# Performance work log

Hardware: AMD Instinct MI355X
Metric: run time of the kernel (lower is better)

The kernel has to match this reference:

```python
import jax, jax.numpy as jnp
import numpy as np

N_HEAD = 16

def setup_inputs() -> dict:
    key = jax.random.key(0)
    kx, kq, kk, kv, kp = jax.random.split(key, 5)
    B, T, C = 4, 2048, 1024
    scale = 1.0 / np.sqrt(C)
    x = jax.random.normal(kx, (B, T, C), dtype=jnp.float32)
    Wq = jax.random.normal(kq, (C, C), dtype=jnp.float32) * scale
    Wk = jax.random.normal(kk, (C, C), dtype=jnp.float32) * scale
    Wv = jax.random.normal(kv, (C, C), dtype=jnp.float32) * scale
    Wp = jax.random.normal(kp, (C, C), dtype=jnp.float32) * scale
    return {"x": x, "Wq": Wq, "Wk": Wk, "Wv": Wv, "Wp": Wp}

def reference(x, Wq, Wk, Wv, Wp):
    B, T, C = x.shape
    H = N_HEAD
    D = C // H
    # projections (nn.Linear, no bias): x @ W^T
    q = (x @ Wq.T).reshape(B, T, H, D).transpose(0, 2, 1, 3)  # [B,H,T,D]
    k = (x @ Wk.T).reshape(B, T, H, D).transpose(0, 2, 1, 3)
    v = (x @ Wv.T).reshape(B, T, H, D).transpose(0, 2, 1, 3)
    att = jnp.einsum('bhqd,bhkd->bhqk', q, k) / jnp.sqrt(jnp.float32(D))
    causal = jnp.tril(jnp.ones((T, T), dtype=bool))
    att = jnp.where(causal, att, -jnp.inf)
    att = jax.nn.softmax(att, axis=-1)
    # dropout p=0.0 -> identity
    y = jnp.einsum('bhqk,bhkd->bhqd', att, v)  # [B,H,T,D]
    y = y.transpose(0, 2, 1, 3).reshape(B, T, C)
    return y @ Wp.T
```

## Files before the change

kernel.cpp:

```cpp
#include <hip/hip_runtime.h>

typedef __bf16 bfrag __attribute__((ext_vector_type(8)));
typedef __bf16 bh4 __attribute__((ext_vector_type(4)));
typedef float f4 __attribute__((ext_vector_type(4)));

#define AS1C(p) (const __attribute__((address_space(1))) void*)(p)
#define AS3(p)  (__attribute__((address_space(3))) void*)(p)

#define QSCALE 0.18033688011112042f

__device__ __forceinline__ void g2l16(const __bf16* g, __bf16* l) {
  __builtin_amdgcn_global_load_lds(AS1C(g), AS3(l), 16, 0, 0);
}

__global__ __launch_bounds__(256) void cvt5(
    const float* __restrict__ s0, const float* __restrict__ s1,
    const float* __restrict__ s2, const float* __restrict__ s3,
    const float* __restrict__ s4,
    __bf16* __restrict__ d0, __bf16* __restrict__ d1, __bf16* __restrict__ d2,
    __bf16* __restrict__ d3, __bf16* __restrict__ d4, long n0, long n1) {
  const float* s; __bf16* d; long n;
  switch (blockIdx.y) {
    case 0: s = s0; d = d0; n = n0; break;
    case 1: s = s1; d = d1; n = n1; break;
    case 2: s = s2; d = d2; n = n1; break;
    case 3: s = s3; d = d3; n = n1; break;
    default: s = s4; d = d4; n = n1; break;
  }
  long i = ((long)blockIdx.x * 256 + threadIdx.x) * 8;
  if (i >= n) return;
  float4 a = *(const float4*)(s + i);
  float4 b = *(const float4*)(s + i + 4);
  bfrag o;
  o[0] = (__bf16)a.x; o[1] = (__bf16)a.y; o[2] = (__bf16)a.z; o[3] = (__bf16)a.w;
  o[4] = (__bf16)b.x; o[5] = (__bf16)b.y; o[6] = (__bf16)b.z; o[7] = (__bf16)b.w;
  *(bfrag*)(d + i) = o;
}

#define BARR __builtin_amdgcn_s_barrier()
#define WAIT_LGKM { asm volatile("s_waitcnt lgkmcnt(0)" ::: "memory"); \
                    __builtin_amdgcn_sched_barrier(0); }
#define WAIT_VM(N) asm volatile("s_waitcnt vmcnt(" #N ")" ::: "memory")

template <int MODE>
__global__ __launch_bounds__(512, 2) void gemm_dp(
    const __bf16* __restrict__ A, const __bf16* __restrict__ Bw,
    __bf16* __restrict__ qb, __bf16* __restrict__ kb,
    __bf16* __restrict__ vt, float* __restrict__ Cf, int K) {
  __shared__ __bf16 lds[73728];
  __bf16* ldsA = lds;
  __bf16* ldsB = lds + 24576;
  const int tid = threadIdx.x;
  const int wave = tid >> 6, lane = tid & 63;
  const int lm = lane & 15, quad = lane >> 4;
  const int wm = wave >> 2, wn = wave & 3;
  const int bm = blockIdx.x * 128, bn = blockIdx.y * 256;
  const int srow = lane >> 3;
  const int scol = ((lane & 7) ^ srow) * 8;
  const int rsw = lm & 7;

#define STG_A9(sl, kt) { \
    const __bf16* gp_ = A + (long)(bm + wave * 16 + srow) * K + (kt) * 64 + scol; \
    __bf16* lp_ = ldsA + (sl) * 8192 + wave * 1024 + lane * 8; \
    g2l16(gp_, lp_); g2l16(gp_ + 8 * K, lp_ + 512); }
#define STG_B9(sl, kt, h) { \
    const __bf16* gp_ = Bw + (long)(bn + (h) * 128 + wave * 16 + srow) * K + (kt) * 64 + scol; \
    __bf16* lp_ = ldsB + (sl) * 16384 + (h) * 8192 + wave * 1024 + lane * 8; \
    g2l16(gp_, lp_); g2l16(gp_ + 8 * K, lp_ + 512); }
#define STG_TILE(sl, kt) { STG_A9(sl, kt); STG_B9(sl, kt, 0); STG_B9(sl, kt, 1); }

#define COMPUTE_HALF(sl) { \
    const __bf16* Ab_ = ldsA + (sl) * 8192 + (wm * 64 + lm) * 64; \
    const __bf16* Bb_ = ldsB + (sl) * 16384 + (wn * 64 + lm) * 64; \
    bfrag af_[4][2], bg_[2][2]; \
    _Pragma("unroll") for (int j_ = 0; j_ < 4; ++j_) \
      _Pragma("unroll") for (int kk_ = 0; kk_ < 2; ++kk_) \
        af_[j_][kk_] = *(const bfrag*)(Ab_ + j_ * 1024 + ((kk_ * 4 + quad) ^ rsw) * 8); \
    _Pragma("unroll") for (int n_ = 0; n_ < 2; ++n_) \
      _Pragma("unroll") for (int kk_ = 0; kk_ < 2; ++kk_) \
        bg_[n_][kk_] = *(const bfrag*)(Bb_ + n_ * 1024 + ((kk_ * 4 + quad) ^ rsw) * 8); \
    WAIT_LGKM; \
    __builtin_amdgcn_s_setprio(1); \
    _Pragma("unroll") for (int j_ = 0; j_ < 4; ++j_) \
      _Pragma("unroll") for (int n_ = 0; n_ < 2; ++n_) \
        _Pragma("unroll") for (int kk_ = 0; kk_ < 2; ++kk_) \
          acc[j_][n_] = __builtin_amdgcn_mfma_f32_16x16x32_bf16( \
              af_[j_][kk_], bg_[n_][kk_], acc[j_][n_], 0, 0, 0); \
    __builtin_amdgcn_s_setprio(0); \
    _Pragma("unroll") for (int n_ = 0; n_ < 2; ++n_) \
      _Pragma("unroll") for (int kk_ = 0; kk_ < 2; ++kk_) \
        bg_[n_][kk_] = *(const bfrag*)(Bb_ + (2 + n_) * 1024 + ((kk_ * 4 + quad) ^ rsw) * 8); \
    WAIT_LGKM; \
    __builtin_amdgcn_s_setprio(1); \
    _Pragma("unroll") for (int j_ = 0; j_ < 4; ++j_) \
      _Pragma("unroll") for (int n_ = 0; n_ < 2; ++n_) \
        _Pragma("unroll") for (int kk_ = 0; kk_ < 2; ++kk_) \
          acc[j_][2 + n_] = __builtin_amdgcn_mfma_f32_16x16x32_bf16( \
              af_[j_][kk_], bg_[n_][kk_], acc[j_][2 + n_], 0, 0, 0); \
    __builtin_amdgcn_s_setprio(0); }

  f4 acc[4][4] = {};
  const int ntiles = K >> 6;
  STG_TILE(0, 0);
  STG_TILE(1, 1);
  WAIT_VM(6);
  BARR;
#pragma unroll 1
  for (int i = 0; i < (ntiles >> 1); ++i) {
    const int e = 2 * i, o = 2 * i + 1;
    const int se = e % 3, so = o % 3;
    if (e + 2 < ntiles) { const int s2 = (e + 2) % 3; STG_TILE(s2, e + 2); }
    COMPUTE_HALF(se);
    if (e + 2 < ntiles) { WAIT_VM(6); } else { WAIT_VM(0); }
    BARR;
    if (o + 2 < ntiles) { const int s2 = (o + 2) % 3; STG_TILE(s2, o + 2); }
    COMPUTE_HALF(so);
    if (o + 2 < ntiles) WAIT_VM(6);
    BARR;
  }

  if (MODE == 1) {
#pragma unroll
    for (int mi = 0; mi < 4; ++mi)
#pragma unroll
      for (int ni = 0; ni < 4; ++ni)
#pragma unroll
        for (int r = 0; r < 4; ++r) {
          long row = bm + wm * 64 + mi * 16 + quad * 4 + r;
          long col = bn + wn * 64 + ni * 16 + lm;
          Cf[row * 1024 + col] = acc[mi][ni][r];
        }
  } else if (bn < 2048) {
    __bf16* dst = (bn < 1024) ? qb : kb;
    const float scl = (bn < 1024) ? QSCALE : 1.0f;
    const int nb = bn & 1023;
#pragma unroll
    for (int mi = 0; mi < 4; ++mi)
#pragma unroll
      for (int ni = 0; ni < 4; ++ni)
#pragma unroll
        for (int r = 0; r < 4; ++r) {
          long row = bm + wm * 64 + mi * 16 + quad * 4 + r;
          long col = nb + wn * 64 + ni * 16 + lm;
          dst[row * 1024 + col] = (__bf16)(acc[mi][ni][r] * scl);
        }
  } else {
#pragma unroll
    for (int mi = 0; mi < 4; ++mi)
#pragma unroll
      for (int ni = 0; ni < 4; ++ni)
#pragma unroll
        for (int r = 0; r < 4; ++r) {
          int d = wn * 64 + ni * 16 + lm;
          int tp = wm * 64 + (quad * 4 + r) * 4 + mi;
          lds[d * 130 + tp] = (__bf16)acc[mi][ni][r];
        }
    __syncthreads();
    const int bloc = bm >> 11;
    const int tloc = bm & 2047;
#pragma unroll
    for (int p = 0; p < 8; ++p) {
      int d = (tid >> 4) + p * 32;
      int c = (tid & 15) * 8;
      long dglob = (bn - 2048) + d;
      *(bfrag*)(vt + ((long)bloc * 1024 + dglob) * 2048 + tloc + c) =
          *(const bfrag*)(lds + d * 130 + c);
    }
  }
}

template <bool A_F32, bool OUT_F32>
__global__ __launch_bounds__(256) void gemm_bt_cv(
    const void* __restrict__ Ap, const float* __restrict__ Bp,
    void* __restrict__ Cp, int M, int N, int K, float scl) {
  __shared__ __bf16 As[128 * 32];
  __shared__ __bf16 Bs[128 * 32];
  const int tid = threadIdx.x;
  const int lane = tid & 63, wave = tid >> 6;
  const int lm = lane & 15, quad = lane >> 4;
  const int bm = blockIdx.x * 128, bn = blockIdx.y * 128;
  const int wr = (wave >> 1) * 64, wc = (wave & 1) * 64;
  const int e0 = tid * 16, sr = e0 >> 5, sc = e0 & 31;
  f4 acc[4][4] = {};
  for (int k0 = 0; k0 < K; k0 += 32) {
    if (A_F32) {
      const float4* ga = (const float4*)((const float*)Ap + (long)(bm + sr) * K + k0 + sc);
#pragma unroll
      for (int j = 0; j < 4; ++j) {
        float4 v = ga[j];
        As[sr * 32 + sc + j * 4 + 0] = (__bf16)v.x;
        As[sr * 32 + sc + j * 4 + 1] = (__bf16)v.y;
        As[sr * 32 + sc + j * 4 + 2] = (__bf16)v.z;
        As[sr * 32 + sc + j * 4 + 3] = (__bf16)v.w;
      }
    } else {
      const __bf16* Ab = (const __bf16*)Ap + (long)(bm + sr) * K + k0 + sc;
      *(bfrag*)(As + sr * 32 + sc) = *(const bfrag*)Ab;
      *(bfrag*)(As + sr * 32 + sc + 8) = *(const bfrag*)(Ab + 8);
    }
    {
      const float4* gb = (const float4*)(Bp + (long)(bn + sr) * K + k0 + sc);
#pragma unroll
      for (int j = 0; j < 4; ++j) {
        float4 v = gb[j];
        Bs[sr * 32 + sc + j * 4 + 0] = (__bf16)v.x;
        Bs[sr * 32 + sc + j * 4 + 1] = (__bf16)v.y;
        Bs[sr * 32 + sc + j * 4 + 2] = (__bf16)v.z;
        Bs[sr * 32 + sc + j * 4 + 3] = (__bf16)v.w;
      }
    }
    __syncthreads();
    bfrag af[4], bg[4];
#pragma unroll
    for (int mi = 0; mi < 4; ++mi)
      af[mi] = *(const bfrag*)(As + (wr + mi * 16 + lm) * 32 + quad * 8);
#pragma unroll
    for (int ni = 0; ni < 4; ++ni)
      bg[ni] = *(const bfrag*)(Bs + (wc + ni * 16 + lm) * 32 + quad * 8);
#pragma unroll
    for (int mi = 0; mi < 4; ++mi)
#pragma unroll
      for (int ni = 0; ni < 4; ++ni)
        acc[mi][ni] = __builtin_amdgcn_mfma_f32_16x16x32_bf16(af[mi], bg[ni], acc[mi][ni], 0, 0, 0);
    __syncthreads();
  }
#pragma unroll
  for (int mi = 0; mi < 4; ++mi)
#pragma unroll
    for (int ni = 0; ni < 4; ++ni)
#pragma unroll
      for (int r = 0; r < 4; ++r) {
        long row = bm + wr + mi * 16 + quad * 4 + r;
        long col = bn + wc + ni * 16 + lm;
        if (OUT_F32) ((float*)Cp)[row * N + col] = acc[mi][ni][r] * scl;
        else ((__bf16*)Cp)[row * N + col] = (__bf16)(acc[mi][ni][r] * scl);
      }
}

template <bool VT>
__global__ __launch_bounds__(256, 2) void attn_fwd10(
    const __bf16* Qg, const __bf16* __restrict__ Kg,
    const __bf16* __restrict__ Vsrc, __bf16* Yg) {
  const int TT = 2048, CC = 1024;
  __shared__ __bf16 Ks[64 * 64];
  __shared__ __bf16 Vs[64 * 64];
  __shared__ __bf16 Ps[16 * 16 * 64];
  const int tid = threadIdx.x;
  const int wave = tid >> 6, lane = tid & 63;
  const int lm = lane & 15, quad = lane >> 4;
  const int bh = blockIdx.x, i = blockIdx.y;
  const int b = bh >> 4, h = bh & 15;
  const int qtA = i, qtB = 15 - i;
  const long rbase = (long)b * TT;
  const int hoff = h * 64;
  int row0[4];
  row0[0] = qtA * 128 + wave * 16;
  row0[1] = qtA * 128 + 64 + wave * 16;
  row0[2] = qtB * 128 + wave * 16;
  row0[3] = qtB * 128 + 64 + wave * 16;
  __bf16* Pw[4];
#pragma unroll
  for (int fr = 0; fr < 4; ++fr) Pw[fr] = Ps + (wave * 4 + fr) * 1024;
  bfrag qf[4][2];
#pragma unroll
  for (int fr = 0; fr < 4; ++fr)
#pragma unroll
    for (int f = 0; f < 2; ++f)
      qf[fr][f] = *(const bfrag*)(Qg + (rbase + row0[fr] + lm) * CC + hoff + f * 32 + quad * 8);
  bfrag ones;
#pragma unroll
  for (int j = 0; j < 8; ++j) ones[j] = (__bf16)1.0f;
  f4 y[4][4] = {};
  f4 L[4] = {};

  const int psl = ((tid & 7) ^ ((tid >> 3) & 7)) * 8;
  const int rsw = lm & 7;

  const int ktLast = 2 * qtB + 1;
  bfrag kin[2], vin[2];
#pragma unroll
  for (int s = 0; s < 2; ++s) {
    int idx = tid + s * 256;
    int r = idx >> 3, c = (idx & 7) * 8;
    kin[s] = *(const bfrag*)(Kg + (rbase + r) * CC + hoff + c);
    if (VT)
      vin[s] = *(const bfrag*)(Vsrc + ((long)b * 1024 + hoff + r) * 2048 + c);
    else
      vin[s] = *(const bfrag*)(Vsrc + (rbase + r) * CC + hoff + c);
  }

  for (int kt = 0; kt <= ktLast; ++kt) {
    const int kBase = kt * 64;
    __syncthreads();
#pragma unroll
    for (int s = 0; s < 2; ++s) {
      int idx = tid + s * 256;
      int r = idx >> 3, c = (idx & 7) * 8;
      *(bfrag*)(Ks + r * 64 + psl) = kin[s];
      if (VT) {
        *(bfrag*)(Vs + r * 64 + psl) = vin[s];
      } else {
        int kp = (r & 15) * 4 + (r >> 4);
#pragma unroll
        for (int j = 0; j < 8; ++j)
          Vs[(c + j) * 64 + ((kp >> 3) ^ ((c + j) & 7)) * 8 + (kp & 7)] = vin[s][j];
      }
    }
    const bool more = (kt < ktLast);
    bfrag kin2[2], vin2[2];
    if (more) {
      const int nB = kBase + 64;
#pragma unroll
      for (int s = 0; s < 2; ++s) {
        int idx = tid + s * 256;
        int r = idx >> 3, c = (idx & 7) * 8;
        kin2[s] = *(const bfrag*)(Kg + (rbase + nB + r) * CC + hoff + c);
        if (VT)
          vin2[s] = *(const bfrag*)(Vsrc + ((long)b * 1024 + hoff + r) * 2048 + nB + c);
        else
          vin2[s] = *(const bfrag*)(Vsrc + (rbase + nB + r) * CC + hoff + c);
      }
    }
    __syncthreads();
    bfrag kf[8];
#pragma unroll
    for (int sub = 0; sub < 4; ++sub)
#pragma unroll
      for (int f = 0; f < 2; ++f)
        kf[sub * 2 + f] = *(const bfrag*)(Ks + (sub * 16 + lm) * 64 + ((f * 4 + quad) ^ rsw) * 8);
#pragma unroll
    for (int fr = 0; fr < 4; ++fr) {
      if (kBase <= row0[fr] + 15) {
        f4 sac[4];
#pragma unroll
        for (int sub = 0; sub < 4; ++sub) {
          f4 z = {};
#pragma unroll
          for (int f = 0; f < 2; ++f)
            z = __builtin_amdgcn_mfma_f32_16x16x32_bf16(qf[fr][f], kf[sub * 2 + f], z, 0, 0, 0);
          sac[sub] = z;
        }
        if (kBase + 63 > row0[fr]) {
#pragma unroll
          for (int r = 0; r < 4; ++r) {
            int prow = quad * 4 + r;
            bh4 pk;
#pragma unroll
            for (int sub = 0; sub < 4; ++sub) {
              float pv = __builtin_amdgcn_exp2f(sac[sub][r]);
              bool masked = (kBase + sub * 16 + lm > row0[fr] + prow);
              pk[sub] = (__bf16)(masked ? 0.f : pv);
            }
            *(bh4*)(Pw[fr] + prow * 64 + ((lm >> 1) ^ (prow & 7)) * 8 + (lm & 1) * 4) = pk;
          }
        } else {
#pragma unroll
          for (int r = 0; r < 4; ++r) {
            int prow = quad * 4 + r;
            bh4 pk;
#pragma unroll
            for (int sub = 0; sub < 4; ++sub)
              pk[sub] = (__bf16)__builtin_amdgcn_exp2f(sac[sub][r]);
            *(bh4*)(Pw[fr] + prow * 64 + ((lm >> 1) ^ (prow & 7)) * 8 + (lm & 1) * 4) = pk;
          }
        }
      }
    }
    __asm__ volatile("s_waitcnt lgkmcnt(0)" ::: "memory");
    bfrag vf[8];
#pragma unroll
    for (int sub = 0; sub < 4; ++sub)
#pragma unroll
      for (int f = 0; f < 2; ++f)
        vf[sub * 2 + f] = *(const bfrag*)(Vs + (sub * 16 + lm) * 64 + ((f * 4 + quad) ^ rsw) * 8);
#pragma unroll
    for (int fr = 0; fr < 4; ++fr) {
      if (kBase <= row0[fr] + 15) {
#pragma unroll
        for (int f = 0; f < 2; ++f) {
          bfrag pf = *(const bfrag*)(Pw[fr] + lm * 64 + ((f * 4 + quad) ^ rsw) * 8);
          L[fr] = __builtin_amdgcn_mfma_f32_16x16x32_bf16(pf, ones, L[fr], 0, 0, 0);
#pragma unroll
          for (int ds = 0; ds < 4; ++ds)
            y[fr][ds] = __builtin_amdgcn_mfma_f32_16x16x32_bf16(pf, vf[ds * 2 + f], y[fr][ds], 0, 0, 0);
        }
      }
    }
    if (more) {
      kin[0] = kin2[0]; kin[1] = kin2[1];
      vin[0] = vin2[0]; vin[1] = vin2[1];
    }
  }
#pragma unroll
  for (int fr = 0; fr < 4; ++fr)
#pragma unroll
    for (int ds = 0; ds < 4; ++ds)
#pragma unroll
      for (int r = 0; r < 4; ++r) {
        long row = rbase + row0[fr] + quad * 4 + r;
        Yg[row * CC + hoff + ds * 16 + lm] = (__bf16)(y[fr][ds][r] / L[fr][r]);
      }
}

extern "C" void kernel_launch(void* const* d_in, const int* in_sizes, int n_in,
                              void* d_out, int out_size, void* d_ws, size_t ws_size,
                              hipStream_t stream) {
  (void)in_sizes; (void)n_in; (void)out_size;
  const float* x  = (const float*)d_in[0];
  const float* Wq = (const float*)d_in[1];
  const float* Wk = (const float*)d_in[2];
  const float* Wv = (const float*)d_in[3];
  const float* Wp = (const float*)d_in[4];
  float* out = (float*)d_out;
  const long R = 8192;
  const long BUF = R * 1024;
  const long WN = 1024L * 1024;
  __bf16* qb = (__bf16*)d_ws;
  __bf16* kb = (__bf16*)d_out;
  __bf16* vslot = kb + BUF;
  dim3 blk(256, 1, 1);
  const size_t need = (size_t)(2 * BUF + 4 * WN) * 2;
  if (ws_size >= need) {
    __bf16* xb = qb + BUF;
    __bf16* wqkv = xb + BUF;
    __bf16* wpb = wqkv + 3 * WN;
    cvt5<<<dim3((unsigned)(BUF / (256 * 8)), 5, 1), blk, 0, stream>>>(
        x, Wq, Wk, Wv, Wp, xb, wqkv, wqkv + WN, wqkv + 2 * WN, wpb, BUF, WN);
    gemm_dp<0><<<dim3(64, 12, 1), dim3(512, 1, 1), 0, stream>>>(
        xb, wqkv, qb, kb, vslot, nullptr, 1024);
    attn_fwd10<true><<<dim3(64, 8, 1), blk, 0, stream>>>(qb, kb, vslot, qb);
    gemm_dp<1><<<dim3(64, 4, 1), dim3(512, 1, 1), 0, stream>>>(
        qb, wpb, nullptr, nullptr, nullptr, out, 1024);
  } else {
    gemm_bt_cv<true, false><<<dim3(64, 8, 1), blk, 0, stream>>>(x, Wq, qb, 8192, 1024, 1024, QSCALE);
    gemm_bt_cv<true, false><<<dim3(64, 8, 1), blk, 0, stream>>>(x, Wk, kb, 8192, 1024, 1024, 1.0f);
    gemm_bt_cv<true, false><<<dim3(64, 8, 1), blk, 0, stream>>>(x, Wv, vslot, 8192, 1024, 1024, 1.0f);
    attn_fwd10<false><<<dim3(64, 8, 1), blk, 0, stream>>>(qb, kb, vslot, qb);
    gemm_bt_cv<false, true><<<dim3(64, 8, 1), blk, 0, stream>>>(qb, Wp, out, 8192, 1024, 1024, 1.0f);
  }
}
```

Before: 223.7 us.

## Double-buffer K/V tiles in LDS to drop one barrier per iteration

The attention kernel now keeps two LDS buffers for the K and V tiles. While the current tile is consumed, the next tile is written into the other buffer and the global load two tiles ahead is issued. This removes one __syncthreads per key-tile iteration and deepens the prefetch. It doubles the K/V shared memory (32KB for Ps plus 32KB K/V) and adds register-held prefetch data, which could affect occupancy at 2 blocks per CU.

Measured after the change: 230.4 us. +3.0%, slower.

```diff
diff --git a/kernel.cpp b/kernel.cpp
--- a/kernel.cpp
+++ b/kernel.cpp
@@ -238,13 +238,13 @@
 }
 
 template <bool VT>
-__global__ __launch_bounds__(256, 2) void attn_fwd10(
+__global__ __launch_bounds__(256, 2) void attn_fwd14(
     const __bf16* Qg, const __bf16* __restrict__ Kg,
     const __bf16* __restrict__ Vsrc, __bf16* Yg) {
   const int TT = 2048, CC = 1024;
-  __shared__ __bf16 Ks[64 * 64];
-  __shared__ __bf16 Vs[64 * 64];
-  __shared__ __bf16 Ps[16 * 16 * 64];
+  __shared__ __bf16 Ks[2][64 * 64];
+  __shared__ __bf16 Vs[2][64 * 64];
+  __shared__ __bf16 Ps[16 * 1024];
   const int tid = threadIdx.x;
   const int wave = tid >> 6, lane = tid & 63;
   const int lm = lane & 15, quad = lane >> 4;
@@ -277,57 +277,51 @@
   const int rsw = lm & 7;
 
   const int ktLast = 2 * qtB + 1;
+
+#define LOADKV(kt) { \
+    const int nB_ = (kt) * 64; \
+    _Pragma("unroll") for (int s = 0; s < 2; ++s) { \
+      int idx_ = tid + s * 256; \
+      int r_ = idx_ >> 3, c_ = (idx_ & 7) * 8; \
+      kin[s] = *(const bfrag*)(Kg + (rbase + nB_ + r_) * CC + hoff + c_); \
+      if (VT) \
+        vin[s] = *(const bfrag*)(Vsrc + ((long)b * 1024 + hoff + r_) * 2048 + nB_ + c_); \
+      else \
+        vin[s] = *(const bfrag*)(Vsrc + (rbase + nB_ + r_) * CC + hoff + c_); \
+    } }
+
+#define STOREKV(db) { \
+    _Pragma("unroll") for (int s = 0; s < 2; ++s) { \
+      int idx_ = tid + s * 256; \
+      int r_ = idx_ >> 3, c_ = (idx_ & 7) * 8; \
+      *(bfrag*)(Ks[db] + r_ * 64 + psl) = kin[s]; \
+      if (VT) { \
+        *(bfrag*)(Vs[db] + r_ * 64 + psl) = vin[s]; \
+      } else { \
+        int kp_ = (r_ & 15) * 4 + (r_ >> 4); \
+        _Pragma("unroll") for (int j = 0; j < 8; ++j) \
+          Vs[db][(c_ + j) * 64 + ((kp_ >> 3) ^ ((c_ + j) & 7)) * 8 + (kp_ & 7)] = vin[s][j]; \
+      } \
+    } }
+
   bfrag kin[2], vin[2];
-#pragma unroll
-  for (int s = 0; s < 2; ++s) {
-    int idx = tid + s * 256;
-    int r = idx >> 3, c = (idx & 7) * 8;
-    kin[s] = *(const bfrag*)(Kg + (rbase + r) * CC + hoff + c);
-    if (VT)
-      vin[s] = *(const bfrag*)(Vsrc + ((long)b * 1024 + hoff + r) * 2048 + c);
-    else
-      vin[s] = *(const bfrag*)(Vsrc + (rbase + r) * CC + hoff + c);
-  }
+  LOADKV(0);
+  STOREKV(0);
+  LOADKV(1);
+  __syncthreads();
 
   for (int kt = 0; kt <= ktLast; ++kt) {
     const int kBase = kt * 64;
-    __syncthreads();
-#pragma unroll
-    for (int s = 0; s < 2; ++s) {
-      int idx = tid + s * 256;
-      int r = idx >> 3, c = (idx & 7) * 8;
-      *(bfrag*)(Ks + r * 64 + psl) = kin[s];
-      if (VT) {
-        *(bfrag*)(Vs + r * 64 + psl) = vin[s];
-      } else {
-        int kp = (r & 15) * 4 + (r >> 4);
-#pragma unroll
-        for (int j = 0; j < 8; ++j)
-          Vs[(c + j) * 64 + ((kp >> 3) ^ ((c + j) & 7)) * 8 + (kp & 7)] = vin[s][j];
-      }
-    }
-    const bool more = (kt < ktLast);
-    bfrag kin2[2], vin2[2];
-    if (more) {
-      const int nB = kBase + 64;
-#pragma unroll
-      for (int s = 0; s < 2; ++s) {
-        int idx = tid + s * 256;
-        int r = idx >> 3, c = (idx & 7) * 8;
-        kin2[s] = *(const bfrag*)(Kg + (rbase + nB + r) * CC + hoff + c);
-        if (VT)
-          vin2[s] = *(const bfrag*)(Vsrc + ((long)b * 1024 + hoff + r) * 2048 + nB + c);
-        else
-          vin2[s] = *(const bfrag*)(Vsrc + (rbase + nB + r) * CC + hoff + c);
-      }
-    }
-    __syncthreads();
+    const int cur = kt & 1;
+    if (kt) __syncthreads();
     bfrag kf[8];
 #pragma unroll
     for (int sub = 0; sub < 4; ++sub)
 #pragma unroll
       for (int f = 0; f < 2; ++f)
-        kf[sub * 2 + f] = *(const bfrag*)(Ks + (sub * 16 + lm) * 64 + ((f * 4 + quad) ^ rsw) * 8);
+        kf[sub * 2 + f] = *(const bfrag*)(Ks[cur] + (sub * 16 + lm) * 64 + ((f * 4 + quad) ^ rsw) * 8);
+    if (kt < ktLast) STOREKV(cur ^ 1);
+    if (kt + 2 <= ktLast) LOADKV(kt + 2);
 #pragma unroll
     for (int fr = 0; fr < 4; ++fr) {
       if (kBase <= row0[fr] + 15) {
@@ -372,7 +366,7 @@
     for (int sub = 0; sub < 4; ++sub)
 #pragma unroll
       for (int f = 0; f < 2; ++f)
-        vf[sub * 2 + f] = *(const bfrag*)(Vs + (sub * 16 + lm) * 64 + ((f * 4 + quad) ^ rsw) * 8);
+        vf[sub * 2 + f] = *(const bfrag*)(Vs[cur] + (sub * 16 + lm) * 64 + ((f * 4 + quad) ^ rsw) * 8);
 #pragma unroll
     for (int fr = 0; fr < 4; ++fr) {
       if (kBase <= row0[fr] + 15) {
@@ -386,10 +380,6 @@
         }
       }
     }
-    if (more) {
-      kin[0] = kin2[0]; kin[1] = kin2[1];
-      vin[0] = vin2[0]; vin[1] = vin2[1];
-    }
   }
 #pragma unroll
   for (int fr = 0; fr < 4; ++fr)
@@ -400,6 +390,8 @@
         long row = rbase + row0[fr] + quad * 4 + r;
         Yg[row * CC + hoff + ds * 16 + lm] = (__bf16)(y[fr][ds][r] / L[fr][r]);
       }
+#undef LOADKV
+#undef STOREKV
 }
 
 extern "C" void kernel_launch(void* const* d_in, const int* in_sizes, int n_in,
@@ -428,14 +420,14 @@
         x, Wq, Wk, Wv, Wp, xb, wqkv, wqkv + WN, wqkv + 2 * WN, wpb, BUF, WN);
     gemm_dp<0><<<dim3(64, 12, 1), dim3(512, 1, 1), 0, stream>>>(
         xb, wqkv, qb, kb, vslot, nullptr, 1024);
-    attn_fwd10<true><<<dim3(64, 8, 1), blk, 0, stream>>>(qb, kb, vslot, qb);
+    attn_fwd14<true><<<dim3(64, 8, 1), blk, 0, stream>>>(qb, kb, vslot, qb);
     gemm_dp<1><<<dim3(64, 4, 1), dim3(512, 1, 1), 0, stream>>>(
         qb, wpb, nullptr, nullptr, nullptr, out, 1024);
   } else {
     gemm_bt_cv<true, false><<<dim3(64, 8, 1), blk, 0, stream>>>(x, Wq, qb, 8192, 1024, 1024, QSCALE);
     gemm_bt_cv<true, false><<<dim3(64, 8, 1), blk, 0, stream>>>(x, Wk, kb, 8192, 1024, 1024, 1.0f);
     gemm_bt_cv<true, false><<<dim3(64, 8, 1), blk, 0, stream>>>(x, Wv, vslot, 8192, 1024, 1024, 1.0f);
-    attn_fwd10<false><<<dim3(64, 8, 1), blk, 0, stream>>>(qb, kb, vslot, qb);
+    attn_fwd14<false><<<dim3(64, 8, 1), blk, 0, stream>>>(qb, kb, vslot, qb);
     gemm_bt_cv<false, true><<<dim3(64, 8, 1), blk, 0, stream>>>(qb, Wp, out, 8192, 1024, 1024, 1.0f);
   }
 }
```
